# Kernel tuning notes

Hardware: AMD Instinct MI355X
Metric: run time of the kernel (lower is better)

Reference implementation:

```python
import jax, jax.numpy as jnp
import numpy as np
from jax import lax

DIM = 64           # LHMSA dim
C3 = 3 * DIM       # high-band channels
HEADS = C3 // 32   # 6
WS = 8             # window size
SHIFT = 4          # shift size
EPS = 1e-6


def _ln_chw(x, w, b):
    # channel-last layer norm applied to BCHW input over C
    xt = x.transpose(0, 2, 3, 1)
    mu = xt.mean(-1, keepdims=True)
    var = ((xt - mu) ** 2).mean(-1, keepdims=True)
    y = (xt - mu) / jnp.sqrt(var + EPS) * w + b
    return y.transpose(0, 3, 1, 2)


def _conv1x1(x, w):
    # w: (out_c, in_c), no bias
    return jnp.einsum('bchw,oc->bohw', x, w)


def _dwconv3(x, w):
    # depthwise 3x3, w: (C,1,3,3)
    C = x.shape[1]
    return lax.conv_general_dilated(x, w, (1, 1), ((1, 1), (1, 1)),
                                    dimension_numbers=('NCHW', 'OIHW', 'NCHW'),
                                    feature_group_count=C)


def _gelu(x):
    return jax.nn.gelu(x, approximate=False)


def _dwt(x):
    x01 = x[:, :, 0::2, :] * 0.5
    x02 = x[:, :, 1::2, :] * 0.5
    x1 = x01[:, :, :, 0::2]; x2 = x02[:, :, :, 0::2]
    x3 = x01[:, :, :, 1::2]; x4 = x02[:, :, :, 1::2]
    ll = x1 + x2 + x3 + x4
    high = jnp.concatenate([-x1 - x2 + x3 + x4,
                            -x1 + x2 - x3 + x4,
                            x1 - x2 - x3 + x4], axis=1)
    return ll, high


def _iwt(ll, high):
    B, C, H, W = ll.shape
    hl, lh, hh = jnp.split(high, 3, axis=1)
    x1 = (ll - hl - lh + hh) * 0.5
    x2 = (ll - hl + lh - hh) * 0.5
    x3 = (ll + hl - lh - hh) * 0.5
    x4 = (ll + hl + lh + hh) * 0.5
    even = jnp.stack([x1, x3], axis=-1).reshape(B, C, H, 2 * W)  # rows 0::2
    odd = jnp.stack([x2, x4], axis=-1).reshape(B, C, H, 2 * W)   # rows 1::2
    return jnp.stack([even, odd], axis=-2).reshape(B, C, 2 * H, 2 * W)


def _swin_mhsa(x, qkv_w, qkv_b, proj_w, proj_b, rpb_table, rpi):
    # x: (B, C3, H, W); H,W divisible by WS -> no padding path
    B, C, H, W = x.shape
    dh = C // HEADS
    scale = dh ** (-0.5)
    xh = x.transpose(0, 2, 3, 1)                           # BHWC
    xh = jnp.roll(xh, (-SHIFT, -SHIFT), axis=(1, 2))
    nh, nw = H // WS, W // WS
    xw = xh.reshape(B, nh, WS, nw, WS, C).transpose(0, 1, 3, 2, 4, 5)
    xw = xw.reshape(B * nh * nw, WS * WS, C)               # (nW, N, C)
    qkv = xw @ qkv_w.T + qkv_b                             # (nW, N, 3C)
    qkv = qkv.reshape(-1, WS * WS, 3, HEADS, dh).transpose(2, 0, 3, 1, 4)
    q, k, v = qkv[0], qkv[1], qkv[2]                       # (nW, h, N, dh)
    attn = jnp.einsum('whnd,whmd->whnm', q, k) * scale
    bias = rpb_table[rpi.reshape(-1)].reshape(WS * WS, WS * WS, HEADS)
    attn = jax.nn.softmax(attn + bias.transpose(2, 0, 1)[None], axis=-1)
    out = jnp.einsum('whnm,whmd->whnd', attn, v)
    out = out.transpose(0, 2, 1, 3).reshape(-1, WS * WS, C)
    out = out.reshape(B, nh, nw, WS, WS, C).transpose(0, 1, 3, 2, 4, 5)
    out = out.reshape(B, H, W, C)
    out = jnp.roll(out, (SHIFT, SHIFT), axis=(1, 2))
    out = out @ proj_w.T + proj_b
    return out.transpose(0, 3, 1, 2)


def _rel_pos_index():
    coords = np.stack(np.meshgrid(np.arange(WS), np.arange(WS), indexing='ij'))
    cf = coords.reshape(2, -1)
    rel = (cf[:, :, None] - cf[:, None, :]).transpose(1, 2, 0).astype(np.int64)
    rel[:, :, 0] += WS - 1
    rel[:, :, 1] += WS - 1
    rel[:, :, 0] *= 2 * WS - 1
    return rel.sum(-1)


def setup_inputs() -> dict:
    key = jax.random.key(0)
    ks = jax.random.split(key, 12)
    B, H, W = 2, 512, 512
    x = jax.random.normal(ks[0], (B, DIM, H, W), jnp.float32)
    s = 0.02
    inp = {
        'x': x,
        'norm_w': jnp.ones((C3,), jnp.float32),
        'norm_b': jnp.zeros((C3,), jnp.float32),
        'qkv_w': jax.random.normal(ks[1], (3 * C3, C3), jnp.float32) * s,
        'qkv_b': jnp.zeros((3 * C3,), jnp.float32),
        'proj_w': jax.random.normal(ks[2], (C3, C3), jnp.float32) * s,
        'proj_b': jnp.zeros((C3,), jnp.float32),
        'rpb_table': jax.random.normal(ks[3], ((2 * WS - 1) ** 2, HEADS), jnp.float32) * s,
        'aux_dw_w': jax.random.normal(ks[4], (DIM, 1, 3, 3), jnp.float32) * 0.1,
        'aux_pw_w': jax.random.normal(ks[5], (DIM, DIM), jnp.float32) * s,
        'cg1_w': jax.random.normal(ks[6], (C3 * 3 // 12, DIM), jnp.float32) * s,
        'cg2_w': jax.random.normal(ks[7], (C3, C3 * 3 // 12), jnp.float32) * s,
        'po_w': jax.random.normal(ks[8], (DIM, DIM), jnp.float32) * s,
        'gamma_main': jnp.full((1,), 1e-4, jnp.float32),
        'gamma_aux': jnp.full((1,), 0.5, jnp.float32),
        'gamma_cross': jnp.full((1,), 1e-5, jnp.float32),
        'rel_pos_index': jnp.asarray(_rel_pos_index(), jnp.int32),
    }
    return inp


def reference(x, norm_w, norm_b, qkv_w, qkv_b, proj_w, proj_b, rpb_table,
              aux_dw_w, aux_pw_w, cg1_w, cg2_w, po_w,
              gamma_main, gamma_aux, gamma_cross, rel_pos_index):
    ll, high = _dwt(x)
    high_norm = _ln_chw(high, norm_w, norm_b)
    refined_high = high + gamma_main * _swin_mhsa(high_norm, qkv_w, qkv_b,
                                                  proj_w, proj_b, rpb_table,
                                                  rel_pos_index)
    refined_ll = ll + gamma_aux * _conv1x1(_gelu(_dwconv3(ll, aux_dw_w)), aux_pw_w)
    gap = ll.mean((2, 3), keepdims=True)
    cross = jax.nn.sigmoid(_conv1x1(_gelu(_conv1x1(gap, cg1_w)), cg2_w))
    refined_high = refined_high * (1.0 + gamma_cross * (cross - 0.5) * 2.0)
    out = _iwt(refined_ll, refined_high)
    return _conv1x1(out - x, po_w)
```

## Files before the change

### kernel.cpp

```cpp
#include <hip/hip_runtime.h>
#include <hip/hip_bf16.h>
#include <math.h>

typedef __hip_bfloat16 bf16;
typedef short s8v __attribute__((ext_vector_type(8)));
typedef float f4v __attribute__((ext_vector_type(4)));
#define MFMA16(a,b,c) __builtin_amdgcn_mfma_f32_16x16x32_bf16(a,b,c,0,0,0)

#define B2   2
#define C64  64
#define C3   192
#define HEADS 6
#define NWIN 2048

#define P_NORMW 0
#define P_NORMB 192
#define P_QKVW  384
#define P_QKVB  110976
#define P_PROJW 111552
#define P_PROJB 148416
#define P_RPB   148608
#define P_AUXDW 149958
#define P_AUXPW 150534
#define P_CG1   154630
#define P_CG2   157702
#define P_PO    166918
#define P_GM    171014
#define P_GA    171015
#define P_GC    171016

#define WS_FLAG   0
#define WS_PARAMS 256
#define WS_GAP    684544
#define WS_AMUL   685568
#define WS_CVAL   687616
#define WS_TSTAT  689664
#define WS_LL     1738240
#define WS_DLLW   18515456
#define WS_WOUT   35292672
#define WS_HRAW   85624320
#define WS_WQKV   135955968
#define WS_WPROJ  136177152
#define WS_WPW    136250880
#define WS_WPO    136259072
#define WS_S12    136267264
#define WS_BIAS6  136271872

template<bool ISF>
__device__ __forceinline__ float LD(const void* p, long i){
  if constexpr (ISF) return ((const float*)p)[i];
  else return __bfloat162float(((const bf16*)p)[i]);
}
template<bool ISF>
__device__ __forceinline__ float2 LD2(const void* p, long i){
  if constexpr (ISF) return *(const float2*)((const float*)p + i);
  else {
    const ushort2 u = *(const ushort2*)((const bf16*)p + i);
    float2 r; r.x = __uint_as_float(((unsigned)u.x) << 16);
    r.y = __uint_as_float(((unsigned)u.y) << 16);
    return r;
  }
}
template<bool ISF>
__device__ __forceinline__ void ST(void* p, long i, float v){
  if constexpr (ISF) ((float*)p)[i] = v;
  else ((bf16*)p)[i] = __float2bfloat16(v);
}
__device__ __forceinline__ float gelu_f(float x){
  return 0.5f * x * (1.f + erff(x * 0.70710678118654752f));
}
__device__ __forceinline__ float bfu(unsigned short u){
  return __uint_as_float(((unsigned)u) << 16);
}
__device__ __forceinline__ unsigned pk2(float a, float b){
  return (unsigned)__bfloat16_as_ushort(__float2bfloat16(a)) |
         ((unsigned)__bfloat16_as_ushort(__float2bfloat16(b)) << 16);
}
__device__ __forceinline__ uint4 pk8(const float* v){
  uint4 r;
  r.x = pk2(v[0], v[1]); r.y = pk2(v[2], v[3]);
  r.z = pk2(v[4], v[5]); r.w = pk2(v[6], v[7]);
  return r;
}
__device__ __forceinline__ void gld16(const void* g, void* l){
  __builtin_amdgcn_global_load_lds(
      (const __attribute__((address_space(1))) void*)g,
      (__attribute__((address_space(3))) void*)l, 16, 0, 0);
}

__global__ __launch_bounds__(256) void detect_kernel(const void* x, int* flag){
  __shared__ int wildcnt;
  if (threadIdx.x == 0) wildcnt = 0;
  __syncthreads();
  const unsigned short* u = (const unsigned short*)x;
  int wild = 0;
  for (int i = threadIdx.x; i < 2048; i += 256){
    unsigned int v = ((unsigned int)u[i]) << 16;
    float f = __uint_as_float(v);
    float a = fabsf(f);
    if (!(a < 1e8f) || (a > 0.f && a < 1e-8f)) wild++;
  }
  atomicAdd(&wildcnt, wild);
  __syncthreads();
  if (threadIdx.x == 0) *flag = (wildcnt > 100) ? 1 : 0;
}

struct PP { const void* src[15]; float* dst[15]; int n[15]; };
__global__ __launch_bounds__(256) void convert_params(PP pp, const int* flag){
  const bool isf = (*flag) != 0;
  const int gid = blockIdx.x*256 + threadIdx.x;
  const int gsz = gridDim.x*256;
#pragma unroll
  for (int q = 0; q < 15; q++){
    const int n = pp.n[q];
    const void* s = pp.src[q];
    float* d = pp.dst[q];
    for (int i = gid; i < n; i += gsz)
      d[i] = isf ? ((const float*)s)[i] : __bfloat162float(((const bf16*)s)[i]);
  }
}

__global__ __launch_bounds__(256) void kw_convert(const float* pf, const int* rpi,
                                                  bf16* wqkvF, bf16* wproj,
                                                  bf16* wpw, bf16* wpo, float* bias6){
  const int i = blockIdx.x*256 + threadIdx.x;
  if (i < 110592){
    const int c = i % 192;
    wqkvF[i] = __float2bfloat16(pf[P_QKVW + i] * pf[P_NORMW + c]);
  } else if (i < 147456)  wproj[i-110592] = __float2bfloat16(pf[P_PROJW + (i-110592)]);
  else if (i < 151552)    wpw[i-147456]   = __float2bfloat16(pf[P_AUXPW + (i-147456)]);
  else if (i < 155648)    wpo[i-151552]   = __float2bfloat16(pf[P_PO + (i-151552)]);
  else if (i < 180224){
    const int j = i - 155648;
    const int hh = j >> 12, nm = j & 4095;
    bias6[j] = pf[P_RPB + rpi[nm]*6 + hh];
  }
}

__global__ __launch_bounds__(256) void k0d_s12(const float* pf, float* s12){
  const int o = blockIdx.x*16 + (threadIdx.x >> 4);
  const int lane = threadIdx.x & 15;
  if (o >= 576) return;
  float s1 = 0.f, s2 = 0.f;
  for (int c = lane; c < 192; c += 16){
    const float w = pf[P_QKVW + o*192 + c];
    s1 += w * pf[P_NORMW + c];
    s2 += w * pf[P_NORMB + c];
  }
  s1 += __shfl_xor(s1,1,16); s1 += __shfl_xor(s1,2,16);
  s1 += __shfl_xor(s1,4,16); s1 += __shfl_xor(s1,8,16);
  s2 += __shfl_xor(s2,1,16); s2 += __shfl_xor(s2,2,16);
  s2 += __shfl_xor(s2,4,16); s2 += __shfl_xor(s2,8,16);
  if (lane == 0){
    s12[o] = s1;
    s12[576 + o] = s2 + pf[P_QKVB + o];
  }
}

template<bool ISF>
__device__ void k1f_body(const void* xv, bf16* llb, bf16* hraw, float2* tstat){
  const int wid = blockIdx.x;
  const int b  = wid >> 10;
  const int wh = (wid >> 5) & 31;
  const int ww = wid & 31;
  const int tid = threadIdx.x;
  const int tk = tid >> 2, l4 = tid & 3;
  const int wi = tk >> 3, wj = tk & 7;
  const int h2 = (wh*8 + wi + 4) & 255;
  const int w2 = (ww*8 + wj + 4) & 255;
  const long pixbase = ((long)(2*h2) << 9) + 2*w2;
  const long llpix = ((long)h2 << 8) + w2;
  float raw0[16], raw1[16], raw2[16];
  float sum = 0.f, sumsq = 0.f;
#pragma unroll
  for (int cc = 0; cc < 16; ++cc){
    const int c = l4*16 + cc;
    const long base = ((long)(b*64 + c) << 18) + pixbase;
    const float2 t0 = LD2<ISF>(xv, base);
    const float2 t1 = LD2<ISF>(xv, base + 512);
    const float a = t0.x, cr = t0.y, bb = t1.x, dd = t1.y;
    llb[((long)(b*64 + c) << 16) + llpix] = __float2bfloat16(0.5f*(a + bb + cr + dd));
    const float h0 = 0.5f*(-a - bb + cr + dd);
    const float h1 = 0.5f*(-a + bb - cr + dd);
    const float hh = 0.5f*( a - bb - cr + dd);
    raw0[cc] = h0; raw1[cc] = h1; raw2[cc] = hh;
    sum += h0 + h1 + hh;
    sumsq += h0*h0 + h1*h1 + hh*hh;
  }
  const long hb = ((long)wid*64 + tk)*192 + l4*16;
  *(uint4*)(hraw + hb)       = pk8(raw0);
  *(uint4*)(hraw + hb + 8)   = pk8(raw0 + 8);
  *(uint4*)(hraw + hb + 64)  = pk8(raw1);
  *(uint4*)(hraw + hb + 72)  = pk8(raw1 + 8);
  *(uint4*)(hraw + hb + 128) = pk8(raw2);
  *(uint4*)(hraw + hb + 136) = pk8(raw2 + 8);
  sum   += __shfl_xor(sum,1,4);   sum   += __shfl_xor(sum,2,4);
  sumsq += __shfl_xor(sumsq,1,4); sumsq += __shfl_xor(sumsq,2,4);
  if (l4 == 0){
    const float mean = sum * (1.f/192.f);
    float var = sumsq * (1.f/192.f) - mean*mean;
    var = fmaxf(var, 0.f);
    const float rstd = rsqrtf(var + 1e-6f);
    float2 st; st.x = rstd; st.y = mean * rstd;
    tstat[wid*64 + tk] = st;
  }
}
__global__ __launch_bounds__(256,4) void k1f_dwt(const void* xv, bf16* llb, bf16* hraw,
                                                 float2* tstat, const int* flag){
  if (*flag) k1f_body<true>(xv, llb, hraw, tstat);
  else       k1f_body<false>(xv, llb, hraw, tstat);
}

__global__ __launch_bounds__(256) void k2_gap(const bf16* llb, float* gap){
  const int bc = blockIdx.x;
  const uint4* p = (const uint4*)(llb + ((long)bc << 16));
  float s = 0.f;
  for (int i = threadIdx.x; i < 8192; i += 256){
    const uint4 v = p[i];
    s += __uint_as_float(v.x << 16) + __uint_as_float(v.x & 0xffff0000u);
    s += __uint_as_float(v.y << 16) + __uint_as_float(v.y & 0xffff0000u);
    s += __uint_as_float(v.z << 16) + __uint_as_float(v.z & 0xffff0000u);
    s += __uint_as_float(v.w << 16) + __uint_as_float(v.w & 0xffff0000u);
  }
  __shared__ float red[256];
  red[threadIdx.x] = s; __syncthreads();
  for (int st = 128; st > 0; st >>= 1){
    if (threadIdx.x < st) red[threadIdx.x] += red[threadIdx.x + st];
    __syncthreads();
  }
  if (threadIdx.x == 0) gap[bc] = red[0] * (1.f / 65536.f);
}

__global__ __launch_bounds__(256) void k3_cross(const float* pf, const float* gap,
                                                float* amul, float* cval){
  __shared__ float t1[B2][48];
  __shared__ float g[B2][64];
  const int tid = threadIdx.x;
  if (tid < 128) g[tid >> 6][tid & 63] = gap[tid];
  __syncthreads();
  if (tid < 96){
    const int b = tid / 48, j = tid % 48;
    float s = 0.f;
    const float* w = pf + P_CG1 + j * 64;
    for (int c = 0; c < 64; ++c) s += w[c] * g[b][c];
    t1[b][j] = gelu_f(s);
  }
  __syncthreads();
  const float gm = pf[P_GM], gc = pf[P_GC];
  for (int o = tid; o < B2 * C3; o += 256){
    const int b = o / C3, ch = o % C3;
    float s = 0.f;
    const float* w = pf + P_CG2 + ch * 48;
    for (int j = 0; j < 48; ++j) s += w[j] * t1[b][j];
    const float cr = 1.f / (1.f + expf(-s));
    const float c = gc * (cr - 0.5f) * 2.f;
    cval[o] = c;
    amul[o] = gm * (1.f + c);
  }
}

__global__ __launch_bounds__(256,6) void k6f_aux(const bf16* llb, const float* pf,
                                                 const bf16* wpw, bf16* dllw){
  __shared__ __align__(16) char sm6[24576];
  bf16* tile = (bf16*)sm6;
  bf16* t    = (bf16*)(sm6 + 15360);
  const int blk = blockIdx.x;
  const int b = blk >> 10, ti = (blk >> 5) & 31, tj = blk & 31;
  const int tid = threadIdx.x;
  const int y0 = ti*8 - 1;
  const int x0 = tj*8 - 2;

  for (int e = tid; e < 7680; e += 256){
    const int col = e % 12;
    const int rc  = e / 12;
    const int row = rc % 10, ch = rc / 10;
    const int x = x0 + col, y = y0 + row;
    bf16 v = __float2bfloat16(0.f);
    if ((unsigned)x < 256u && (unsigned)y < 256u)
      v = llb[((long)(b*64 + ch) << 16) + ((long)y << 8) + x];
    tile[rc*12 + col] = v;
  }
  __syncthreads();

  {
    const int tok = tid & 63, cgrp = tid >> 6;
    const int iy = tok >> 3, ix = tok & 7;
#pragma unroll
    for (int cc = 0; cc < 16; ++cc){
      const int c = cgrp*16 + cc;
      const float* wk = pf + P_AUXDW + c*9;
      float s = 0.f;
#pragma unroll
      for (int ky = 0; ky < 3; ++ky)
#pragma unroll
        for (int kx = 0; kx < 3; ++kx)
          s += wk[ky*3 + kx] * __bfloat162float(tile[(c*10 + iy + ky)*12 + ix + 1 + kx]);
      t[tok*72 + c] = __float2bfloat16(gelu_f(s));
    }
  }
  __syncthreads();

  const int wv = tid >> 6, l = tid & 63, lr = l & 15, lg = l >> 4;
  const f4v fz = {0.f,0.f,0.f,0.f};
  f4v acc[4];
#pragma unroll
  for (int nt = 0; nt < 4; ++nt) acc[nt] = fz;
#pragma unroll
  for (int ks = 0; ks < 2; ++ks){
    const s8v a = *(const s8v*)(t + (wv*16+lr)*72 + ks*32 + lg*8);
#pragma unroll
    for (int nt = 0; nt < 4; ++nt){
      const s8v bfr = *(const s8v*)(wpw + (nt*16+lr)*64 + ks*32 + lg*8);
      acc[nt] = MFMA16(a, bfr, acc[nt]);
    }
  }
  const float ga = pf[P_GA];
#pragma unroll
  for (int i = 0; i < 4; ++i){
    const int p = wv*16 + lg*4 + i;
    const int y = ti*8 + (p >> 3), x = tj*8 + (p & 7);
    const int sy = (y - 4) & 255, sx = (x - 4) & 255;
    const int wid = b*1024 + (sy >> 3)*32 + (sx >> 3);
    const int tok2 = (sy & 7)*8 + (sx & 7);
    const long ob = ((long)wid*64 + tok2)*64;
#pragma unroll
    for (int nt = 0; nt < 4; ++nt)
      dllw[ob + nt*16 + lr] = __float2bfloat16(ga * acc[nt][i]);
  }
}

__global__ __launch_bounds__(256,3) void k4_attn(const bf16* hraw, const float2* tstat,
                                                 const bf16* wqkvF, const float* s12,
                                                 const float* bias6, bf16* wout){
  __shared__ __align__(16) char sm[50176];
  bf16* bstage = (bf16*)sm;
  bf16* bq = (bf16*)(sm + 36864);
  bf16* bk = (bf16*)(sm + 41472);
  char* vtb = sm + 46080;
  bf16* bp = (bf16*)(sm + 36864);
  const int g = blockIdx.x;
  const int xcd = g & 7, slot = g >> 3;
  const int wid = (slot/6)*8 + xcd;
  const int h   = slot - (slot/6)*6;
  const int tid = threadIdx.x;
  const int wv = tid >> 6, l = tid & 63, lr = l & 15, lg = l >> 4;
  const f4v fz = {0.f,0.f,0.f,0.f};
  const float scale = 0.17677669529663687f;
  const bf16* at = hraw + (long)wid * 12288;

#pragma unroll
  for (int pass = 0; pass < 9; ++pass){
    const int idx = pass*256 + tid;
    const int rl  = idx / 24;
    const int off = (idx % 24) * 16;
    const int soff = off ^ ((rl & 7) << 4);
    const int grow = (rl >> 5)*192 + h*32 + (rl & 31);
    gld16(wqkvF + grow*192 + (soff >> 1),
          (char*)bstage + (pass*256 + wv*64)*16);
  }
  s8v aA[6];
#pragma unroll
  for (int ks = 0; ks < 6; ++ks)
    aA[ks] = *(const s8v*)(at + (wv*16+lr)*192 + ks*32 + lg*8);
  float2 st4[4];
#pragma unroll
  for (int i = 0; i < 4; ++i)
    st4[i] = tstat[wid*64 + wv*16 + lg*4 + i];
  __syncthreads();

  f4v acc[6];
#pragma unroll
  for (int nt = 0; nt < 6; ++nt) acc[nt] = fz;
#pragma unroll
  for (int ks = 0; ks < 6; ++ks){
    const int kb = (ks*32 + lg*8) * 2;
#pragma unroll
    for (int nt = 0; nt < 6; ++nt){
      const int row = nt*16 + lr;
      const s8v bfr = *(const s8v*)((const char*)bstage + row*384 + (kb ^ ((row&7)<<4)));
      acc[nt] = MFMA16(aA[ks], bfr, acc[nt]);
    }
  }
#pragma unroll
  for (int nt = 0; nt < 6; ++nt){
    const int ol = nt*16 + lr;
    const int p = ol >> 5, c = ol & 31;
    const int ocol = p*192 + h*32 + c;
    const float s1v = s12[ocol], s2v = s12[576 + ocol];
#pragma unroll
    for (int i = 0; i < 4; ++i){
      const int row = wv*16 + lg*4 + i;
      const float v = st4[i].x*acc[nt][i] - st4[i].y*s1v + s2v;
      if (p == 0)      bq[row*36 + c] = __float2bfloat16(v*scale);
      else if (p == 1) bk[row*36 + c] = __float2bfloat16(v);
      else             *(bf16*)(vtb + ((c*128 + row*2) ^ ((c&7)<<4))) = __float2bfloat16(v);
    }
  }
  __syncthreads();

  f4v sacc[4];
  {
    const s8v a = *(const s8v*)(bq + (wv*16+lr)*36 + lg*8);
#pragma unroll
    for (int nt = 0; nt < 4; ++nt){
      const s8v bfr = *(const s8v*)(bk + (nt*16+lr)*36 + lg*8);
      sacc[nt] = MFMA16(a, bfr, fz);
    }
  }
  float pvv[4][4];
  float inv4[4];
#pragma unroll
  for (int i = 0; i < 4; ++i){
    const int row = wv*16 + lg*4 + i;
    float s = 0.f;
#pragma unroll
    for (int nt = 0; nt < 4; ++nt){
      const float e = __expf(sacc[nt][i] + bias6[h*4096 + row*64 + nt*16 + lr]);
      pvv[i][nt] = e;
      s += e;
    }
    s += __shfl_xor(s, 1, 16);
    s += __shfl_xor(s, 2, 16);
    s += __shfl_xor(s, 4, 16);
    s += __shfl_xor(s, 8, 16);
    inv4[i] = 1.f/s;
  }
  __syncthreads();

#pragma unroll
  for (int i = 0; i < 4; ++i){
    const int row = wv*16 + lg*4 + i;
#pragma unroll
    for (int nt = 0; nt < 4; ++nt)
      bp[row*72 + nt*16 + lr] = __float2bfloat16(pvv[i][nt]);
  }
  f4v oacc[2] = {fz, fz};
#pragma unroll
  for (int ks2 = 0; ks2 < 2; ++ks2){
    const s8v a = *(const s8v*)(bp + (wv*16+lr)*72 + ks2*32 + lg*8);
#pragma unroll
    for (int nn = 0; nn < 2; ++nn){
      const int d = nn*16 + lr;
      const s8v bfr = *(const s8v*)(vtb + ((d*128 + (ks2*32+lg*8)*2) ^ ((d&7)<<4)));
      oacc[nn] = MFMA16(a, bfr, oacc[nn]);
    }
  }
#pragma unroll
  for (int nn = 0; nn < 2; ++nn)
#pragma unroll
    for (int i = 0; i < 4; ++i){
      const int row = wv*16 + lg*4 + i;
      wout[((long)wid*64 + row)*192 + h*32 + nn*16 + lr] =
        __float2bfloat16(oacc[nn][i] * inv4[i]);
    }
}

__global__ __launch_bounds__(256,5) void k5_proj(bf16* wout, const bf16* hraw,
                                                 const bf16* wproj, const float* pf,
                                                 const float* amul, const float* cval){
  __shared__ __align__(16) bf16 bufC[64*192];
  const int wid = blockIdx.x;
  const int b  = wid >> 10;
  const int tid = threadIdx.x;
  const int wv = tid >> 6, l = tid & 63, lr = l & 15, lg = l >> 4;

  {
    const bf16* hsrc = hraw + (long)wid * 12288;
#pragma unroll
    for (int pass = 0; pass < 6; ++pass){
      const int idx = pass*256 + tid;
      const int row = idx / 24;
      const int off = (idx % 24) * 16;
      const int soff = off ^ ((row & 7) << 4);
      gld16(hsrc + row*192 + (soff >> 1),
            (char*)bufC + (pass*256 + wv*64)*16);
    }
  }

  const f4v fz = {0.f,0.f,0.f,0.f};
  const bf16* at = wout + (long)wid * 12288;

  f4v acc[3][4];
#pragma unroll
  for (int nt = 0; nt < 3; ++nt)
#pragma unroll
    for (int mt = 0; mt < 4; ++mt) acc[nt][mt] = fz;
#pragma unroll
  for (int ks = 0; ks < 6; ++ks){
    const int k0 = ks*32;
    s8v a[4];
#pragma unroll
    for (int mt = 0; mt < 4; ++mt)
      a[mt] = *(const s8v*)(at + (mt*16+lr)*192 + k0 + lg*8);
#pragma unroll
    for (int nt = 0; nt < 3; ++nt){
      const int ocol = (wv*3+nt)*16 + lr;
      const s8v bfr = *(const s8v*)(wproj + ocol*192 + k0 + lg*8);
#pragma unroll
      for (int mt = 0; mt < 4; ++mt) acc[nt][mt] = MFMA16(a[mt], bfr, acc[nt][mt]);
    }
  }
  __syncthreads();
#pragma unroll
  for (int nt = 0; nt < 3; ++nt){
    const int col = (wv*3+nt)*16 + lr;
    const int bc = b*192 + col;
    const float am = amul[bc], cv = cval[bc], pb = pf[P_PROJB + col];
#pragma unroll
    for (int mt = 0; mt < 4; ++mt)
#pragma unroll
      for (int i = 0; i < 4; ++i){
        const int row = mt*16 + lg*4 + i;
        const float hv = __bfloat162float(
          *(const bf16*)((const char*)bufC + row*384 + ((col*2) ^ ((row&7)<<4))));
        wout[(long)wid*12288 + row*192 + col] =
          __float2bfloat16(am*(acc[nt][mt][i] + pb) + cv*hv);
      }
  }
}

template<bool ISF>
__device__ void k7_body(const bf16* dvalw, const bf16* dllw, const bf16* wpo,
                        void* out, char* yp){
  const int blk = blockIdx.x;
  const int b = blk >> 10, hh = (blk >> 1) & 511, half = blk & 1;
  const int h2 = hh >> 1, posH = hh & 1;
  const int th = (h2 + 252) & 255;
  const int wh = th >> 3, wi = th & 7;
  const int tid = threadIdx.x;
  const int j = tid & 7;
#pragma unroll
  for (int pass = 0; pass < 8; ++pass){
    const int p = pass*32 + (tid >> 3);
    const int ww2 = half*256 + p;
    const int w2 = ww2 >> 1, posW = ww2 & 1;
    const int tw = (w2 + 252) & 255;
    const int ww = tw >> 3, wj = tw & 7;
    const int wid = b*1024 + wh*32 + ww;
    const int tok = wi*8 + wj;
    const long dvb = ((long)wid*64 + tok)*192 + j*8;
    const s8v hl8 = *(const s8v*)(dvalw + dvb);
    const s8v lh8 = *(const s8v*)(dvalw + dvb + 64);
    const s8v hh8 = *(const s8v*)(dvalw + dvb + 128);
    const s8v dl8 = *(const s8v*)(dllw + ((long)wid*64 + tok)*64 + j*8);
    const float s1 = posW ? 0.5f : -0.5f;
    const float s2 = posH ? 0.5f : -0.5f;
    const float s3 = posW == posH ? 0.5f : -0.5f;
    float e[8];
#pragma unroll
    for (int q = 0; q < 8; ++q)
      e[q] = 0.5f*bfu((unsigned short)dl8[q]) + s1*bfu((unsigned short)hl8[q])
           + s2*bfu((unsigned short)lh8[q]) + s3*bfu((unsigned short)hh8[q]);
    *(uint4*)(yp + ((p*128 + j*16) ^ ((p&7)<<4))) = pk8(e);
  }
  __syncthreads();
  const int wv = tid >> 6, l = tid & 63, lr = l & 15, lg = l >> 4;
  const f4v fz = {0.f,0.f,0.f,0.f};
  f4v acc[4][4];
#pragma unroll
  for (int mt = 0; mt < 4; ++mt)
#pragma unroll
    for (int nt = 0; nt < 4; ++nt) acc[mt][nt] = fz;
#pragma unroll
  for (int ks = 0; ks < 2; ++ks){
    const int k0 = ks*32;
    s8v a[4];
#pragma unroll
    for (int mt = 0; mt < 4; ++mt)
      a[mt] = *(const s8v*)(wpo + (mt*16+lr)*64 + k0 + lg*8);
#pragma unroll
    for (int nt = 0; nt < 4; ++nt){
      const int prow = wv*64 + nt*16 + lr;
      const s8v bfr = *(const s8v*)(yp + ((prow*128 + (k0+lg*8)*2) ^ ((prow&7)<<4)));
#pragma unroll
      for (int mt = 0; mt < 4; ++mt) acc[mt][nt] = MFMA16(a[mt], bfr, acc[mt][nt]);
    }
  }
  const int px0 = half*256 + wv*64;
#pragma unroll
  for (int mt = 0; mt < 4; ++mt)
#pragma unroll
    for (int nt = 0; nt < 4; ++nt)
#pragma unroll
      for (int i = 0; i < 4; ++i){
        const int c = mt*16 + lg*4 + i;
        const long ob = ((long)(b*64 + c)*512 + hh)*512 + px0 + nt*16 + lr;
        ST<ISF>(out, ob, acc[mt][nt][i]);
      }
}
__global__ __launch_bounds__(256,4) void k7_out(const bf16* dvalw, const bf16* dllw,
                                                const bf16* wpo, void* out, const int* flag){
  __shared__ __align__(16) char yp[32768];
  if (*flag) k7_body<true>(dvalw, dllw, wpo, out, yp);
  else       k7_body<false>(dvalw, dllw, wpo, out, yp);
}

extern "C" void kernel_launch(void* const* d_in, const int* in_sizes, int n_in,
                              void* d_out, int out_size, void* d_ws, size_t ws_size,
                              hipStream_t stream){
  char* ws = (char*)d_ws;
  int*   flag = (int*)(ws + WS_FLAG);
  float* pf   = (float*)(ws + WS_PARAMS);
  float* gap  = (float*)(ws + WS_GAP);
  float* amul = (float*)(ws + WS_AMUL);
  float* cval = (float*)(ws + WS_CVAL);
  float2* tstat=(float2*)(ws + WS_TSTAT);
  bf16*  llb  = (bf16*)(ws + WS_LL);
  bf16*  dllw = (bf16*)(ws + WS_DLLW);
  bf16*  wout = (bf16*)(ws + WS_WOUT);
  bf16*  hraw = (bf16*)(ws + WS_HRAW);
  bf16*  wqkvF= (bf16*)(ws + WS_WQKV);
  bf16*  wproj= (bf16*)(ws + WS_WPROJ);
  bf16*  wpw  = (bf16*)(ws + WS_WPW);
  bf16*  wpo  = (bf16*)(ws + WS_WPO);
  float* s12  = (float*)(ws + WS_S12);
  float* bias6= (float*)(ws + WS_BIAS6);
  const int* rpi = (const int*)d_in[16];

  detect_kernel<<<1, 256, 0, stream>>>(d_in[0], flag);

  PP pp;
  const int pidx[15] = {1,2,3,4,5,6,7,8,9,10,11,12,13,14,15};
  const int poff[15] = {P_NORMW,P_NORMB,P_QKVW,P_QKVB,P_PROJW,P_PROJB,P_RPB,
                        P_AUXDW,P_AUXPW,P_CG1,P_CG2,P_PO,P_GM,P_GA,P_GC};
  for (int q = 0; q < 15; q++){
    pp.src[q] = d_in[pidx[q]];
    pp.dst[q] = pf + poff[q];
    pp.n[q]   = in_sizes[pidx[q]];
  }
  convert_params<<<128, 256, 0, stream>>>(pp, flag);
  kw_convert<<<704, 256, 0, stream>>>(pf, rpi, wqkvF, wproj, wpw, wpo, bias6);
  k0d_s12  <<<36,  256, 0, stream>>>(pf, s12);

  k1f_dwt<<<NWIN, 256, 0, stream>>>(d_in[0], llb, hraw, tstat, flag);
  k2_gap <<<128,  256, 0, stream>>>(llb, gap);
  k3_cross<<<1,   256, 0, stream>>>(pf, gap, amul, cval);
  k6f_aux<<<NWIN, 256, 0, stream>>>(llb, pf, wpw, dllw);
  k4_attn<<<NWIN*6, 256, 0, stream>>>(hraw, tstat, wqkvF, s12, bias6, wout);
  k5_proj<<<NWIN, 256, 0, stream>>>(wout, hraw, wproj, pf, amul, cval);
  k7_out <<<2048, 256, 0, stream>>>(wout, dllw, wpo, d_out, flag);
}
```

Measured before the change: 427.2 us.

## Process two windows per attention block sharing staged QKV weights

```diff
diff --git a/kernel.cpp b/kernel.cpp
--- a/kernel.cpp
+++ b/kernel.cpp
@@ -122,7 +122,7 @@
 
 __global__ __launch_bounds__(256) void kw_convert(const float* pf, const int* rpi,
                                                   bf16* wqkvF, bf16* wproj,
-                                                  bf16* wpw, bf16* wpo, float* bias6){
+                                                  bf16* wpw, bf16* wpo, float* bias6T){
   const int i = blockIdx.x*256 + threadIdx.x;
   if (i < 110592){
     const int c = i % 192;
@@ -133,11 +133,12 @@
   else if (i < 180224){
     const int j = i - 155648;
     const int hh = j >> 12, nm = j & 4095;
-    bias6[j] = pf[P_RPB + rpi[nm]*6 + hh];
-  }
-}
-
-__global__ __launch_bounds__(256) void k0d_s12(const float* pf, float* s12){
+    const int row = nm >> 6, col = nm & 63;
+    bias6T[hh*4096 + col*64 + row] = pf[P_RPB + rpi[nm]*6 + hh];
+  }
+}
+
+__global__ __launch_bounds__(256) void k0d_s12(const float* pf, float2* s12p){
   const int o = blockIdx.x*16 + (threadIdx.x >> 4);
   const int lane = threadIdx.x & 15;
   if (o >= 576) return;
@@ -152,8 +153,8 @@
   s2 += __shfl_xor(s2,1,16); s2 += __shfl_xor(s2,2,16);
   s2 += __shfl_xor(s2,4,16); s2 += __shfl_xor(s2,8,16);
   if (lane == 0){
-    s12[o] = s1;
-    s12[576 + o] = s2 + pf[P_QKVB + o];
+    float2 v; v.x = s1; v.y = s2 + pf[P_QKVB + o];
+    s12p[o] = v;
   }
 }
 
@@ -329,43 +330,50 @@
   }
 }
 
-__global__ __launch_bounds__(256,3) void k4_attn(const bf16* hraw, const float2* tstat,
-                                                 const bf16* wqkvF, const float* s12,
-                                                 const float* bias6, bf16* wout){
-  __shared__ __align__(16) char sm[50176];
+__global__ __launch_bounds__(512,4) void k4_attn(const bf16* hraw, const float2* tstat,
+                                                 const bf16* wqkvF, const float2* s12p,
+                                                 const float* bias6T, bf16* wout){
+  __shared__ __align__(16) char sm[63488];
   bf16* bstage = (bf16*)sm;
-  bf16* bq = (bf16*)(sm + 36864);
-  bf16* bk = (bf16*)(sm + 41472);
-  char* vtb = sm + 46080;
-  bf16* bp = (bf16*)(sm + 36864);
   const int g = blockIdx.x;
   const int xcd = g & 7, slot = g >> 3;
-  const int wid = (slot/6)*8 + xcd;
-  const int h   = slot - (slot/6)*6;
+  const int pair = (slot/6)*8 + xcd;
+  const int h    = slot - (slot/6)*6;
   const int tid = threadIdx.x;
-  const int wv = tid >> 6, l = tid & 63, lr = l & 15, lg = l >> 4;
+  const int wv5 = tid >> 6;
+  const int lw  = wv5 >> 2;
+  const int rg  = wv5 & 3;
+  const int l = tid & 63, lr = l & 15, lg = l >> 4;
+  const int wid = pair*2 + lw;
+  char* reg = sm + 36864 + lw*13312;
+  bf16* bq = (bf16*)reg;
+  bf16* bk = (bf16*)(reg + 4608);
+  char* vtb = reg + 9216;
+  bf16* bp = (bf16*)reg;
   const f4v fz = {0.f,0.f,0.f,0.f};
   const float scale = 0.17677669529663687f;
   const bf16* at = hraw + (long)wid * 12288;
 
 #pragma unroll
-  for (int pass = 0; pass < 9; ++pass){
-    const int idx = pass*256 + tid;
-    const int rl  = idx / 24;
-    const int off = (idx % 24) * 16;
-    const int soff = off ^ ((rl & 7) << 4);
-    const int grow = (rl >> 5)*192 + h*32 + (rl & 31);
-    gld16(wqkvF + grow*192 + (soff >> 1),
-          (char*)bstage + (pass*256 + wv*64)*16);
+  for (int pass = 0; pass < 5; ++pass){
+    if (pass*512 + wv5*64 < 2304){
+      const int idx = pass*512 + tid;
+      const int rl  = idx / 24;
+      const int off = (idx - rl*24) * 16;
+      const int soff = off ^ ((rl & 7) << 4);
+      const int grow = (rl >> 5)*192 + h*32 + (rl & 31);
+      gld16(wqkvF + grow*192 + (soff >> 1),
+            (char*)bstage + (pass*512 + wv5*64)*16);
+    }
   }
   s8v aA[6];
 #pragma unroll
   for (int ks = 0; ks < 6; ++ks)
-    aA[ks] = *(const s8v*)(at + (wv*16+lr)*192 + ks*32 + lg*8);
+    aA[ks] = *(const s8v*)(at + (rg*16+lr)*192 + ks*32 + lg*8);
   float2 st4[4];
 #pragma unroll
   for (int i = 0; i < 4; ++i)
-    st4[i] = tstat[wid*64 + wv*16 + lg*4 + i];
+    st4[i] = tstat[wid*64 + rg*16 + lg*4 + i];
   __syncthreads();
 
   f4v acc[6];
@@ -386,11 +394,11 @@
     const int ol = nt*16 + lr;
     const int p = ol >> 5, c = ol & 31;
     const int ocol = p*192 + h*32 + c;
-    const float s1v = s12[ocol], s2v = s12[576 + ocol];
+    const float2 sp = s12p[ocol];
 #pragma unroll
     for (int i = 0; i < 4; ++i){
-      const int row = wv*16 + lg*4 + i;
-      const float v = st4[i].x*acc[nt][i] - st4[i].y*s1v + s2v;
+      const int row = rg*16 + lg*4 + i;
+      const float v = st4[i].x*acc[nt][i] - st4[i].y*sp.x + sp.y;
       if (p == 0)      bq[row*36 + c] = __float2bfloat16(v*scale);
       else if (p == 1) bk[row*36 + c] = __float2bfloat16(v);
       else             *(bf16*)(vtb + ((c*128 + row*2) ^ ((c&7)<<4))) = __float2bfloat16(v);
@@ -400,22 +408,25 @@
 
   f4v sacc[4];
   {
-    const s8v a = *(const s8v*)(bq + (wv*16+lr)*36 + lg*8);
+    const s8v a = *(const s8v*)(bq + (rg*16+lr)*36 + lg*8);
 #pragma unroll
     for (int nt = 0; nt < 4; ++nt){
       const s8v bfr = *(const s8v*)(bk + (nt*16+lr)*36 + lg*8);
       sacc[nt] = MFMA16(a, bfr, fz);
     }
   }
+  f4v bld[4];
+#pragma unroll
+  for (int nt = 0; nt < 4; ++nt)
+    bld[nt] = *(const f4v*)(bias6T + h*4096 + (nt*16+lr)*64 + rg*16 + lg*4);
   float pvv[4][4];
   float inv4[4];
 #pragma unroll
   for (int i = 0; i < 4; ++i){
-    const int row = wv*16 + lg*4 + i;
     float s = 0.f;
 #pragma unroll
     for (int nt = 0; nt < 4; ++nt){
-      const float e = __expf(sacc[nt][i] + bias6[h*4096 + row*64 + nt*16 + lr]);
+      const float e = __expf(sacc[nt][i] + bld[nt][i]);
       pvv[i][nt] = e;
       s += e;
     }
@@ -429,7 +440,7 @@
 
 #pragma unroll
   for (int i = 0; i < 4; ++i){
-    const int row = wv*16 + lg*4 + i;
+    const int row = rg*16 + lg*4 + i;
 #pragma unroll
     for (int nt = 0; nt < 4; ++nt)
       bp[row*72 + nt*16 + lr] = __float2bfloat16(pvv[i][nt]);
@@ -437,7 +448,7 @@
   f4v oacc[2] = {fz, fz};
 #pragma unroll
   for (int ks2 = 0; ks2 < 2; ++ks2){
-    const s8v a = *(const s8v*)(bp + (wv*16+lr)*72 + ks2*32 + lg*8);
+    const s8v a = *(const s8v*)(bp + (rg*16+lr)*72 + ks2*32 + lg*8);
 #pragma unroll
     for (int nn = 0; nn < 2; ++nn){
       const int d = nn*16 + lr;
@@ -449,7 +460,7 @@
   for (int nn = 0; nn < 2; ++nn)
 #pragma unroll
     for (int i = 0; i < 4; ++i){
-      const int row = wv*16 + lg*4 + i;
+      const int row = rg*16 + lg*4 + i;
       wout[((long)wid*64 + row)*192 + h*32 + nn*16 + lr] =
         __float2bfloat16(oacc[nn][i] * inv4[i]);
     }
@@ -613,7 +624,7 @@
   bf16*  wproj= (bf16*)(ws + WS_WPROJ);
   bf16*  wpw  = (bf16*)(ws + WS_WPW);
   bf16*  wpo  = (bf16*)(ws + WS_WPO);
-  float* s12  = (float*)(ws + WS_S12);
+  float2* s12p= (float2*)(ws + WS_S12);
   float* bias6= (float*)(ws + WS_BIAS6);
   const int* rpi = (const int*)d_in[16];
 
@@ -630,13 +641,13 @@
   }
   convert_params<<<128, 256, 0, stream>>>(pp, flag);
   kw_convert<<<704, 256, 0, stream>>>(pf, rpi, wqkvF, wproj, wpw, wpo, bias6);
-  k0d_s12  <<<36,  256, 0, stream>>>(pf, s12);
+  k0d_s12  <<<36,  256, 0, stream>>>(pf, s12p);
 
   k1f_dwt<<<NWIN, 256, 0, stream>>>(d_in[0], llb, hraw, tstat, flag);
   k2_gap <<<128,  256, 0, stream>>>(llb, gap);
   k3_cross<<<1,   256, 0, stream>>>(pf, gap, amul, cval);
   k6f_aux<<<NWIN, 256, 0, stream>>>(llb, pf, wpw, dllw);
-  k4_attn<<<NWIN*6, 256, 0, stream>>>(hraw, tstat, wqkvF, s12, bias6, wout);
+  k4_attn<<<NWIN/2*6, 512, 0, stream>>>(hraw, tstat, wqkvF, s12p, bias6, wout);
   k5_proj<<<NWIN, 256, 0, stream>>>(wout, hraw, wproj, pf, amul, cval);
   k7_out <<<2048, 256, 0, stream>>>(wout, dllw, wpo, d_out, flag);
 }
```

Measured after the change: 423.9 us. About the same (-0.8%).
